# Kernel optimization log

Hardware: AMD Instinct MI355X
Metric: run time of the kernel (lower is better)

The kernel has to match this reference:

```python
import jax, jax.numpy as jnp
import numpy as np

EPS = 1e-12  # torch F.normalize default eps


def setup_inputs() -> dict:
    key = jax.random.key(0)
    k1, k2, k3, k4, k5 = jax.random.split(key, 5)
    N, E, D_IN, D_OUT = 100000, 1600000, 128, 128
    features = jax.random.normal(k1, (N, D_IN), dtype=jnp.float32)
    W = jax.random.normal(k2, (D_OUT, D_IN), dtype=jnp.float32) * 0.05
    b = jax.random.normal(k3, (D_OUT,), dtype=jnp.float32) * 0.05
    src = jax.random.randint(k4, (E,), 0, N, dtype=jnp.int32)
    dst = jax.random.randint(k5, (E,), 0, N, dtype=jnp.int32)
    return {"features": features, "W": W, "b": b, "src": src, "dst": dst}


def reference(features, W, b, src, dst):
    N = features.shape[0]
    # sum of features over each node's neighbors: scatter-add messages to dst
    neigh_sum = jax.ops.segment_sum(features[src], dst, num_segments=N)  # [N, D]
    total = jnp.sum(features, axis=0)  # [D]
    # non-neighbor sum (excl. self) + self feature == total - neighbor_sum
    h_NN = total[None, :] - neigh_sum  # [N, D]
    # row-wise L2 normalize (torch F.normalize dim=1)
    norm = jnp.sqrt(jnp.sum(h_NN * h_NN, axis=1, keepdims=True))
    h_norm = h_NN / jnp.maximum(norm, EPS)
    # linear: x @ W.T + b
    return h_norm @ W.T + b
```

## Files before the change

### kernel.cpp

```cpp
#include <hip/hip_runtime.h>
#include <hip/hip_bf16.h>

#define D 128
#define FS_CAP 5120

typedef __bf16 bf16_t;
typedef bf16_t bf16x8 __attribute__((ext_vector_type(8)));
typedef float  f32x4  __attribute__((ext_vector_type(4)));
typedef float  f32x2  __attribute__((ext_vector_type(2)));

__device__ __forceinline__ void atomAddF(float* p, float v) {
    unsafeAtomicAdd(p, v);
}

__device__ __forceinline__ uint2 pack_fp8x8(const float* v) {
    unsigned lo = 0, hi = 0;
    lo = __builtin_amdgcn_cvt_pk_fp8_f32(v[0], v[1], lo, false);
    lo = __builtin_amdgcn_cvt_pk_fp8_f32(v[2], v[3], lo, true);
    hi = __builtin_amdgcn_cvt_pk_fp8_f32(v[4], v[5], hi, false);
    hi = __builtin_amdgcn_cvt_pk_fp8_f32(v[6], v[7], hi, true);
    return make_uint2(lo, hi);
}

__device__ __forceinline__ void acc_fp8x8(uint2 w, float* acc) {
    f32x2 a = __builtin_amdgcn_cvt_pk_f32_fp8(w.x, false);
    f32x2 b = __builtin_amdgcn_cvt_pk_f32_fp8(w.x, true);
    f32x2 c = __builtin_amdgcn_cvt_pk_f32_fp8(w.y, false);
    f32x2 d = __builtin_amdgcn_cvt_pk_f32_fp8(w.y, true);
    acc[0] += a[0]; acc[1] += a[1]; acc[2] += b[0]; acc[3] += b[1];
    acc[4] += c[0]; acc[5] += c[1]; acc[6] += d[0]; acc[7] += d[1];
}

__global__ __launch_bounds__(256) void cvt_colsum_count_kernel(const float* __restrict__ feat,
                                                               uint2* __restrict__ featq,
                                                               float* __restrict__ total,
                                                               const int* __restrict__ dst,
                                                               int* __restrict__ bcount,
                                                               int* __restrict__ chunkhist,
                                                               long long n8, int nE, int NB,
                                                               int chunk) {
    __shared__ float red[4][16][8];
    __shared__ int hist[1024];
    int tid = threadIdx.x, lane = tid & 63, w = tid >> 6;
    for (int i = tid; i < NB; i += 256) hist[i] = 0;
    __syncthreads();
    long long G = (long long)gridDim.x * 256;
    float acc[8];
    #pragma unroll
    for (int e = 0; e < 8; ++e) acc[e] = 0.f;
    int c0 = blockIdx.x * chunk;
    int c1 = c0 + chunk; if (c1 > nE) c1 = nE;
    long long i = (long long)blockIdx.x * 256 + tid;
    int e = c0 + tid;
    while (i < n8 || e < c1) {
        if (i < n8) {
            const float4 a = *(const float4*)&feat[i * 8];
            const float4 b = *(const float4*)&feat[i * 8 + 4];
            float v[8] = {a.x, a.y, a.z, a.w, b.x, b.y, b.z, b.w};
            featq[i] = pack_fp8x8(v);
            acc[0] += a.x; acc[1] += a.y; acc[2] += a.z; acc[3] += a.w;
            acc[4] += b.x; acc[5] += b.y; acc[6] += b.z; acc[7] += b.w;
        }
        if (e < c1) atomicAdd(&hist[dst[e] >> 8], 1);
        i += G; e += 256;
    }
    #pragma unroll
    for (int k = 0; k < 8; ++k) {
        acc[k] += __shfl_xor(acc[k], 16, 64);
        acc[k] += __shfl_xor(acc[k], 32, 64);
    }
    if (lane < 16) {
        #pragma unroll
        for (int k = 0; k < 8; ++k) red[w][lane][k] = acc[k];
    }
    __syncthreads();
    if (tid < 128) {
        int cb = tid >> 3, k = tid & 7;
        float s = red[0][cb][k] + red[1][cb][k] + red[2][cb][k] + red[3][cb][k];
        atomAddF(&total[cb * 8 + k], s);
    }
    int* ch = chunkhist + (size_t)blockIdx.x * 1024;
    for (int k = tid; k < NB; k += 256) {
        int h = hist[k];
        ch[k] = h;
        if (h) atomicAdd(&bcount[k], h);
    }
}

__global__ __launch_bounds__(1024) void bscan_kernel(const int* __restrict__ bcount,
                                                     int* __restrict__ bbase,
                                                     int* __restrict__ bcur,
                                                     int NB, int nE) {
    int tid = threadIdx.x, lane = tid & 63, w = tid >> 6;
    int v = (tid < NB) ? bcount[tid] : 0;
    int x = v;
    #pragma unroll
    for (int off = 1; off < 64; off <<= 1) {
        int y = __shfl_up(x, off, 64);
        if (lane >= off) x += y;
    }
    __shared__ int ws[16];
    if (lane == 63) ws[w] = x;
    __syncthreads();
    if (w == 0 && lane < 16) {
        int s = ws[lane];
        #pragma unroll
        for (int off = 1; off < 16; off <<= 1) {
            int y = __shfl_up(s, off, 64);
            if (lane >= off) s += y;
        }
        ws[lane] = s;
    }
    __syncthreads();
    int base = (w == 0) ? 0 : ws[w - 1];
    int excl = base + x - v;
    if (tid < NB) { bbase[tid] = excl; bcur[tid] = excl; }
    if (tid == 0) bbase[NB] = nE;
}

__global__ __launch_bounds__(256) void bucket_scatter_kernel(const int* __restrict__ src,
                                                             const int* __restrict__ dst,
                                                             int* __restrict__ bcur,
                                                             unsigned* __restrict__ packed,
                                                             const int* __restrict__ chunkhist,
                                                             int nE, int NB, int chunk) {
    __shared__ int cur[1024];
    int tid = threadIdx.x;
    const int* ch = chunkhist + (size_t)blockIdx.x * 1024;
    for (int i = tid; i < NB; i += 256) {
        int h = ch[i];
        cur[i] = h ? atomicAdd(&bcur[i], h) : 0;
    }
    __syncthreads();
    int c0 = blockIdx.x * chunk;
    int c1 = c0 + chunk; if (c1 > nE) c1 = nE;
    for (int i = c0 + tid; i < c1; i += 256) {
        int t = dst[i];
        int b = t >> 8;
        int off = atomicAdd(&cur[b], 1);
        packed[off] = ((unsigned)(t & 255) << 17) | (unsigned)src[i];
    }
}

__global__ __launch_bounds__(1024) void fill_sort_kernel(const unsigned* __restrict__ packed,
                                                         const int* __restrict__ bbase,
                                                         int* __restrict__ ptr,
                                                         int* __restrict__ adj,
                                                         int n, int NB, int nE) {
    __shared__ int cnt[256];
    __shared__ int lcur[256];
    __shared__ int wsum[4];
    __shared__ int pbuf[FS_CAP];
    __shared__ int sbuf[FS_CAP];
    int b = blockIdx.x;
    int tid = threadIdx.x, lane = tid & 63, w = tid >> 6;
    int base = bbase[b], end = bbase[b + 1], m = end - base;
    bool fast = (m <= FS_CAP);
    if (tid < 256) cnt[tid] = 0;
    __syncthreads();
    if (fast) {
        for (int i = tid; i < m; i += 1024) {
            int pv = (int)packed[base + i];
            pbuf[i] = pv;
            atomicAdd(&cnt[pv >> 17], 1);
        }
    } else {
        for (int i = tid; i < m; i += 1024)
            atomicAdd(&cnt[packed[base + i] >> 17], 1);
    }
    __syncthreads();
    int v = 0, x = 0;
    if (tid < 256) {
        v = cnt[tid];
        x = v;
        #pragma unroll
        for (int off = 1; off < 64; off <<= 1) {
            int y = __shfl_up(x, off, 64);
            if (lane >= off) x += y;
        }
        if (lane == 63) wsum[w] = x;
    }
    __syncthreads();
    if (tid < 256) {
        int wb = 0;
        for (int k = 0; k < w; ++k) wb += wsum[k];
        int excl = wb + x - v;
        lcur[tid] = fast ? excl : base + excl;
        int node = b * 256 + tid;
        if (node < n) ptr[node] = base + excl;
    }
    if (b == NB - 1 && tid == 0) ptr[n] = nE;
    __syncthreads();
    if (fast) {
        for (int i = tid; i < m; i += 1024) {
            int pv = pbuf[i];
            int j = pv >> 17;
            int pos = atomicAdd(&lcur[j], 1);
            sbuf[pos] = pv & 0x1FFFF;
        }
        __syncthreads();
        for (int i = tid; i < m; i += 1024)
            adj[base + i] = sbuf[i];
    } else {
        for (int i = tid; i < m; i += 1024) {
            int pv = (int)packed[base + i];
            int j = pv >> 17;
            int pos = atomicAdd(&lcur[j], 1);
            adj[pos] = pv & 0x1FFFF;
        }
    }
}

__global__ __launch_bounds__(256, 4) void gather_mfma_kernel(const uint2* __restrict__ featq,
                                                             const int* __restrict__ ptr,
                                                             const int* __restrict__ adj,
                                                             const float* __restrict__ total,
                                                             const float* __restrict__ W,
                                                             const float* __restrict__ bias,
                                                             float* __restrict__ out,
                                                             int n, int ngroups) {
    __shared__ bf16_t s_hn[2][16][136];

    int tid  = threadIdx.x;
    int lane = tid & 63;
    int w    = tid >> 6;
    int quad = lane >> 4;
    int l16  = lane & 15;

    int n0 = w * 32;
    bf16x8 bfrag[4][2];
    #pragma unroll
    for (int s = 0; s < 4; ++s)
        #pragma unroll
        for (int c = 0; c < 2; ++c) {
            const float* wp = W + (size_t)(n0 + 16 * c + l16) * D + 32 * s + 8 * quad;
            float4 wa = *(const float4*)wp;
            float4 wb = *(const float4*)(wp + 4);
            bf16x8 bf;
            bf[0] = (bf16_t)wa.x; bf[1] = (bf16_t)wa.y; bf[2] = (bf16_t)wa.z; bf[3] = (bf16_t)wa.w;
            bf[4] = (bf16_t)wb.x; bf[5] = (bf16_t)wb.y; bf[6] = (bf16_t)wb.z; bf[7] = (bf16_t)wb.w;
            bfrag[s][c] = bf;
        }
    float bias0 = bias[n0 + l16];
    float bias1 = bias[n0 + 16 + l16];

    int k_node = tid >> 4;
    int d8 = (tid & 15) * 8;
    float tot8[8];
    {
        float4 ta = *(const float4*)&total[d8];
        float4 tb = *(const float4*)&total[d8 + 4];
        tot8[0] = ta.x; tot8[1] = ta.y; tot8[2] = ta.z; tot8[3] = ta.w;
        tot8[4] = tb.x; tot8[5] = tb.y; tot8[6] = tb.z; tot8[7] = tb.w;
    }

    unsigned sliceoff = (unsigned)(tid & 15) * 8;
    unsigned long long fbase = (unsigned long long)featq;
    int pb = 0;
    int gstride = gridDim.x;
    int g = blockIdx.x;

    int p0 = 0, p1 = 0, madj = 0;
    if (g < ngroups) {
        int v = g * 16 + k_node;
        if (v < n) { p0 = ptr[v]; p1 = ptr[v + 1]; }
        if (p0 < p1) { int q = p0 + l16; if (q > p1 - 1) q = p1 - 1; madj = adj[q]; }
    }

    for (; g < ngroups; g += gstride) {
        int gn = g + gstride;
        int np0 = 0, np1 = 0;
        if (gn < ngroups) {
            int vn = gn * 16 + k_node;
            if (vn < n) { np0 = ptr[vn]; np1 = ptr[vn + 1]; }
        }

        float acc8[8];
        #pragma unroll
        for (int e = 0; e < 8; ++e) acc8[e] = 0.f;

        for (int p = p0; p < p1; p += 16) {
            int rem = p1 - p;
            unsigned voff[16];
            #pragma unroll
            for (int i = 0; i < 16; ++i) {
                int idx = __shfl(madj, (lane & 48) + i, 64);
                voff[i] = ((unsigned)idx << 7) | sliceoff;
            }
            uint2 f[16];
            #pragma unroll
            for (int i = 0; i < 16; ++i)
                asm volatile("global_load_dwordx2 %0, %1, %2"
                             : "=v"(f[i]) : "v"(voff[i]), "s"(fbase));
            int adjn = 0, pn = p + 16;
            if (pn < p1) { int q = pn + l16; if (q > p1 - 1) q = p1 - 1; adjn = adj[q]; }
            asm volatile("s_waitcnt vmcnt(8)" ::: "memory");
            __builtin_amdgcn_sched_barrier(0);
            #pragma unroll
            for (int i = 0; i < 8; ++i) if (i < rem) acc_fp8x8(f[i], acc8);
            asm volatile("s_waitcnt vmcnt(0)" ::: "memory");
            __builtin_amdgcn_sched_barrier(0);
            #pragma unroll
            for (int i = 8; i < 16; ++i) if (i < rem) acc_fp8x8(f[i], acc8);
            madj = adjn;
        }

        int v = g * 16 + k_node;
        bool valid = v < n;
        float h8[8], ss = 0.f;
        #pragma unroll
        for (int e = 0; e < 8; ++e) {
            h8[e] = valid ? (tot8[e] - acc8[e]) : 0.f;
            ss = fmaf(h8[e], h8[e], ss);
        }
        ss += __shfl_xor(ss, 1, 64);
        ss += __shfl_xor(ss, 2, 64);
        ss += __shfl_xor(ss, 4, 64);
        ss += __shfl_xor(ss, 8, 64);
        float rinv = 1.0f / fmaxf(sqrtf(ss), 1e-12f);

        bf16x8 hv;
        #pragma unroll
        for (int e = 0; e < 8; ++e) hv[e] = (bf16_t)(h8[e] * rinv);
        *(bf16x8*)&s_hn[pb][k_node][d8] = hv;
        __syncthreads();

        p0 = np0; p1 = np1; madj = 0;
        if (p0 < p1) { int q = p0 + l16; if (q > p1 - 1) q = p1 - 1; madj = adj[q]; }

        f32x4 acc0 = {0.f, 0.f, 0.f, 0.f};
        f32x4 acc1 = {0.f, 0.f, 0.f, 0.f};
        #pragma unroll
        for (int s = 0; s < 4; ++s) {
            bf16x8 a = *(const bf16x8*)&s_hn[pb][l16][32 * s + 8 * quad];
            acc0 = __builtin_amdgcn_mfma_f32_16x16x32_bf16(a, bfrag[s][0], acc0, 0, 0, 0);
            acc1 = __builtin_amdgcn_mfma_f32_16x16x32_bf16(a, bfrag[s][1], acc1, 0, 0, 0);
        }
        #pragma unroll
        for (int r = 0; r < 4; ++r) {
            int row = quad * 4 + r;
            int vr = g * 16 + row;
            if (vr < n) {
                out[(size_t)vr * D + n0 + l16]      = acc0[r] + bias0;
                out[(size_t)vr * D + n0 + 16 + l16] = acc1[r] + bias1;
            }
        }
        pb ^= 1;
    }
}

__global__ __launch_bounds__(128) void col_sum_kernel(const float* __restrict__ feat,
                                                      float* __restrict__ total, int n) {
    int d = threadIdx.x;
    float acc = 0.f;
    for (int r = blockIdx.x; r < n; r += gridDim.x)
        acc += feat[(size_t)r * D + d];
    atomAddF(&total[d], acc);
}

__global__ __launch_bounds__(256) void scatter_kernel(const float* __restrict__ feat,
                                                      const int* __restrict__ src,
                                                      const int* __restrict__ dst,
                                                      float* __restrict__ neigh, int nE) {
    long long nwork = (long long)nE * 64;
    long long stride = (long long)gridDim.x * 256;
    for (long long i = (long long)blockIdx.x * 256 + threadIdx.x; i < nwork; i += stride) {
        int e = (int)(i >> 6);
        int d2 = (int)(i & 63) * 2;
        int s = src[e], t = dst[e];
        const float2 vv = *(const float2*)&feat[(size_t)s * D + d2];
        float* p = &neigh[(size_t)t * D + d2];
        atomAddF(p + 0, vv.x);
        atomAddF(p + 1, vv.y);
    }
}

__global__ __launch_bounds__(256) void finalize_kernel(const float* __restrict__ neigh,
                                                       const float* __restrict__ total,
                                                       const float* __restrict__ W,
                                                       const float* __restrict__ bias,
                                                       float* __restrict__ out,
                                                       int n, int ngroups) {
    __shared__ __hip_bfloat16 Wt[D * D];
    __shared__ __align__(16) float hnt[2][D][4];
    __shared__ float red[2][2][4];
    int tid = threadIdx.x;
    for (int idx = tid; idx < D * D; idx += 256) {
        int j = idx & 127, dd = idx >> 7;
        Wt[idx] = __float2bfloat16(W[(size_t)j * D + dd]);
    }
    int half = tid >> 7, d = tid & 127, wih = (tid >> 6) & 1, lane = tid & 63;
    float bj = bias[d], tot = total[d];
    __syncthreads();
    for (int g = blockIdx.x; g < ngroups; g += gridDim.x) {
        int nb = g * 8 + half * 4;
        float h0=0,h1=0,h2=0,h3=0;
        if (nb+0 < n) h0 = tot - neigh[(size_t)(nb+0)*D + d];
        if (nb+1 < n) h1 = tot - neigh[(size_t)(nb+1)*D + d];
        if (nb+2 < n) h2 = tot - neigh[(size_t)(nb+2)*D + d];
        if (nb+3 < n) h3 = tot - neigh[(size_t)(nb+3)*D + d];
        float s0=h0*h0,s1=h1*h1,s2=h2*h2,s3=h3*h3;
        #pragma unroll
        for (int off = 32; off > 0; off >>= 1) {
            s0 += __shfl_xor(s0, off, 64); s1 += __shfl_xor(s1, off, 64);
            s2 += __shfl_xor(s2, off, 64); s3 += __shfl_xor(s3, off, 64);
        }
        if (lane == 0) { red[half][wih][0]=s0; red[half][wih][1]=s1; red[half][wih][2]=s2; red[half][wih][3]=s3; }
        __syncthreads();
        float rinv[4];
        #pragma unroll
        for (int k = 0; k < 4; ++k)
            rinv[k] = 1.0f / fmaxf(sqrtf(red[half][0][k] + red[half][1][k]), 1e-12f);
        hnt[half][d][0]=h0*rinv[0]; hnt[half][d][1]=h1*rinv[1];
        hnt[half][d][2]=h2*rinv[2]; hnt[half][d][3]=h3*rinv[3];
        __syncthreads();
        float a0=0,a1=0,a2=0,a3=0;
        #pragma unroll 8
        for (int dd = 0; dd < D; ++dd) {
            float4 hn4 = *(const float4*)&hnt[half][dd][0];
            float wv = __bfloat162float(Wt[dd * D + d]);
            a0 = fmaf(hn4.x, wv, a0); a1 = fmaf(hn4.y, wv, a1);
            a2 = fmaf(hn4.z, wv, a2); a3 = fmaf(hn4.w, wv, a3);
        }
        if (nb+0 < n) out[(size_t)(nb+0)*D + d] = a0 + bj;
        if (nb+1 < n) out[(size_t)(nb+1)*D + d] = a1 + bj;
        if (nb+2 < n) out[(size_t)(nb+2)*D + d] = a2 + bj;
        if (nb+3 < n) out[(size_t)(nb+3)*D + d] = a3 + bj;
        __syncthreads();
    }
}

static inline size_t align_up(size_t x, size_t a) { return (x + a - 1) & ~(a - 1); }

extern "C" void kernel_launch(void* const* d_in, const int* in_sizes, int n_in,
                              void* d_out, int out_size, void* d_ws, size_t ws_size,
                              hipStream_t stream) {
    const float* feat = (const float*)d_in[0];
    const float* W    = (const float*)d_in[1];
    const float* bias = (const float*)d_in[2];
    const int*   src  = (const int*)d_in[3];
    const int*   dst  = (const int*)d_in[4];
    float* out = (float*)d_out;

    int n  = in_sizes[0] / D;
    int nE = in_sizes[3];
    int NB = (n + 255) / 256;

    char* wsb = (char*)d_ws;
    size_t o_total  = 0;
    size_t o_bcount = 512;
    size_t o_bbase  = 4608;
    size_t o_bcur   = o_bbase + 4608;
    size_t o_chist  = align_up(o_bcur + 4096, 512);
    size_t o_ptr    = o_chist + (size_t)512 * 1024 * 4;
    size_t o_adj    = align_up(o_ptr + (size_t)4 * (n + 1), 512);
    size_t o_packed = o_adj + (size_t)4 * nE;
    size_t o_featq  = align_up(o_packed + (size_t)4 * nE, 512);
    size_t needNew  = o_featq + (size_t)n * D;

    float*    total  = (float*)(wsb + o_total);
    int*      bcount = (int*)(wsb + o_bcount);
    int*      bbase  = (int*)(wsb + o_bbase);
    int*      bcur   = (int*)(wsb + o_bcur);
    int*      chist  = (int*)(wsb + o_chist);
    int*      ptr    = (int*)(wsb + o_ptr);
    int*      adj    = (int*)(wsb + o_adj);
    unsigned* packed = (unsigned*)(wsb + o_packed);
    uint2*    featq  = (uint2*)(wsb + o_featq);

    long long n8 = (long long)n * (D / 8);
    int ngroups16 = (n + 15) / 16;
    int grid16 = (ngroups16 + 2) / 3;
    if (grid16 > 4096) grid16 = 4096;

    bool packOK = (n <= (1 << 17)) && (NB <= 1024);

    if (ws_size >= needNew && packOK) {
        hipMemsetAsync(wsb, 0, o_bbase, stream);
        int chunk = (nE + 511) / 512;
        cvt_colsum_count_kernel<<<512, 256, 0, stream>>>(feat, featq, total, dst, bcount,
                                                         chist, n8, nE, NB, chunk);
        bscan_kernel<<<1, 1024, 0, stream>>>(bcount, bbase, bcur, NB, nE);
        bucket_scatter_kernel<<<512, 256, 0, stream>>>(src, dst, bcur, packed, chist,
                                                       nE, NB, chunk);
        fill_sort_kernel<<<NB, 1024, 0, stream>>>(packed, bbase, ptr, adj, n, NB, nE);
        gather_mfma_kernel<<<grid16, 256, 0, stream>>>(featq, ptr, adj, total, W,
                                                       bias, out, n, ngroups16);
    } else {
        float* neigh = out;
        if (ws_size >= D * sizeof(float))
            hipMemsetAsync(d_ws, 0, D * sizeof(float), stream);
        hipMemsetAsync(neigh, 0, (size_t)out_size * sizeof(float), stream);
        col_sum_kernel<<<512, 128, 0, stream>>>(feat, total, n);
        scatter_kernel<<<16384, 256, 0, stream>>>(feat, src, dst, neigh, nE);
        int ngroups = (n + 7) / 8;
        finalize_kernel<<<2048, 256, 0, stream>>>(neigh, total, W, bias, out, n, ngroups);
    }
}
```

Baseline: 217.8 us.

## Fold bucket prefix scan into scatter kernel and coarsen chunk histograms

Removes the single-block bscan launch by having each of 128 scatter blocks redundantly compute the bucket exclusive scan, with offsets taken from a relative cursor array. Chunk histograms are merged four-to-one with global atomics, so there are 128 larger scatter blocks of 1024 threads instead of 512 of 256. The gather kernel's grid cap and blocks-per-group ratio also change. This saves one launch and its serialization, at the cost of redundant scan work, extra atomics in the count kernel, and a larger memset region.

Result: faster. 211.5 us (-2.9%).

```diff
diff --git a/kernel.cpp b/kernel.cpp
--- a/kernel.cpp
+++ b/kernel.cpp
@@ -38,7 +38,7 @@
                                                                int* __restrict__ bcount,
                                                                int* __restrict__ chunkhist,
                                                                long long n8, int nE, int NB,
-                                                               int chunk) {
+                                                               int echunk) {
     __shared__ float red[4][16][8];
     __shared__ int hist[1024];
     int tid = threadIdx.x, lane = tid & 63, w = tid >> 6;
@@ -48,8 +48,8 @@
     float acc[8];
     #pragma unroll
     for (int e = 0; e < 8; ++e) acc[e] = 0.f;
-    int c0 = blockIdx.x * chunk;
-    int c1 = c0 + chunk; if (c1 > nE) c1 = nE;
+    int c0 = blockIdx.x * echunk;
+    int c1 = c0 + echunk; if (c1 > nE) c1 = nE;
     long long i = (long long)blockIdx.x * 256 + tid;
     int e = c0 + tid;
     while (i < n8 || e < c1) {
@@ -79,19 +79,26 @@
         float s = red[0][cb][k] + red[1][cb][k] + red[2][cb][k] + red[3][cb][k];
         atomAddF(&total[cb * 8 + k], s);
     }
-    int* ch = chunkhist + (size_t)blockIdx.x * 1024;
+    int* ch = chunkhist + (size_t)(blockIdx.x >> 2) * 1024;
     for (int k = tid; k < NB; k += 256) {
         int h = hist[k];
-        ch[k] = h;
-        if (h) atomicAdd(&bcount[k], h);
-    }
-}
-
-__global__ __launch_bounds__(1024) void bscan_kernel(const int* __restrict__ bcount,
-                                                     int* __restrict__ bbase,
-                                                     int* __restrict__ bcur,
-                                                     int NB, int nE) {
+        if (h) { atomicAdd(&ch[k], h); atomicAdd(&bcount[k], h); }
+    }
+}
+
+__global__ __launch_bounds__(1024) void bucket_scatter_kernel(const int* __restrict__ src,
+                                                              const int* __restrict__ dst,
+                                                              const int* __restrict__ bcount,
+                                                              int* __restrict__ bcur_rel,
+                                                              int* __restrict__ bbase,
+                                                              unsigned* __restrict__ packed,
+                                                              const int* __restrict__ chunkhist,
+                                                              int nE, int NB, int echunk4) {
+    __shared__ int ws[16];
+    __shared__ int cur[1024];
+    int blk = blockIdx.x;
     int tid = threadIdx.x, lane = tid & 63, w = tid >> 6;
+
     int v = (tid < NB) ? bcount[tid] : 0;
     int x = v;
     #pragma unroll
@@ -99,7 +106,6 @@
         int y = __shfl_up(x, off, 64);
         if (lane >= off) x += y;
     }
-    __shared__ int ws[16];
     if (lane == 63) ws[w] = x;
     __syncthreads();
     if (w == 0 && lane < 16) {
@@ -114,27 +120,20 @@
     __syncthreads();
     int base = (w == 0) ? 0 : ws[w - 1];
     int excl = base + x - v;
-    if (tid < NB) { bbase[tid] = excl; bcur[tid] = excl; }
-    if (tid == 0) bbase[NB] = nE;
-}
-
-__global__ __launch_bounds__(256) void bucket_scatter_kernel(const int* __restrict__ src,
-                                                             const int* __restrict__ dst,
-                                                             int* __restrict__ bcur,
-                                                             unsigned* __restrict__ packed,
-                                                             const int* __restrict__ chunkhist,
-                                                             int nE, int NB, int chunk) {
-    __shared__ int cur[1024];
-    int tid = threadIdx.x;
-    const int* ch = chunkhist + (size_t)blockIdx.x * 1024;
-    for (int i = tid; i < NB; i += 256) {
-        int h = ch[i];
-        cur[i] = h ? atomicAdd(&bcur[i], h) : 0;
-    }
-    __syncthreads();
-    int c0 = blockIdx.x * chunk;
-    int c1 = c0 + chunk; if (c1 > nE) c1 = nE;
-    for (int i = c0 + tid; i < c1; i += 256) {
+
+    if (blk == 0) {
+        if (tid < NB) bbase[tid] = excl;
+        if (tid == 0) bbase[NB] = nE;
+    }
+    if (tid < NB) {
+        int h = chunkhist[(size_t)blk * 1024 + tid];
+        cur[tid] = h ? (excl + atomicAdd(&bcur_rel[tid], h)) : 0;
+    }
+    __syncthreads();
+
+    int c0 = blk * echunk4;
+    int c1 = c0 + echunk4; if (c1 > nE) c1 = nE;
+    for (int i = c0 + tid; i < c1; i += 1024) {
         int t = dst[i];
         int b = t >> 8;
         int off = atomicAdd(&cur[b], 1);
@@ -449,10 +448,10 @@
     char* wsb = (char*)d_ws;
     size_t o_total  = 0;
     size_t o_bcount = 512;
-    size_t o_bbase  = 4608;
-    size_t o_bcur   = o_bbase + 4608;
-    size_t o_chist  = align_up(o_bcur + 4096, 512);
-    size_t o_ptr    = o_chist + (size_t)512 * 1024 * 4;
+    size_t o_bcurr  = 512 + 4096;
+    size_t o_chist  = o_bcurr + 4096;
+    size_t o_bbase  = o_chist + (size_t)128 * 1024 * 4;
+    size_t o_ptr    = align_up(o_bbase + 4608, 512);
     size_t o_adj    = align_up(o_ptr + (size_t)4 * (n + 1), 512);
     size_t o_packed = o_adj + (size_t)4 * nE;
     size_t o_featq  = align_up(o_packed + (size_t)4 * nE, 512);
@@ -460,9 +459,9 @@
 
     float*    total  = (float*)(wsb + o_total);
     int*      bcount = (int*)(wsb + o_bcount);
+    int*      bcurr  = (int*)(wsb + o_bcurr);
+    int*      chist  = (int*)(wsb + o_chist);
     int*      bbase  = (int*)(wsb + o_bbase);
-    int*      bcur   = (int*)(wsb + o_bcur);
-    int*      chist  = (int*)(wsb + o_chist);
     int*      ptr    = (int*)(wsb + o_ptr);
     int*      adj    = (int*)(wsb + o_adj);
     unsigned* packed = (unsigned*)(wsb + o_packed);
@@ -470,19 +469,19 @@
 
     long long n8 = (long long)n * (D / 8);
     int ngroups16 = (n + 15) / 16;
-    int grid16 = (ngroups16 + 2) / 3;
-    if (grid16 > 4096) grid16 = 4096;
+    int grid16 = (ngroups16 + 1) / 2;
+    if (grid16 > 16384) grid16 = 16384;
 
     bool packOK = (n <= (1 << 17)) && (NB <= 1024);
 
     if (ws_size >= needNew && packOK) {
         hipMemsetAsync(wsb, 0, o_bbase, stream);
-        int chunk = (nE + 511) / 512;
+        int echunk = (nE + 511) / 512;
+        int echunk4 = echunk * 4;
         cvt_colsum_count_kernel<<<512, 256, 0, stream>>>(feat, featq, total, dst, bcount,
-                                                         chist, n8, nE, NB, chunk);
-        bscan_kernel<<<1, 1024, 0, stream>>>(bcount, bbase, bcur, NB, nE);
-        bucket_scatter_kernel<<<512, 256, 0, stream>>>(src, dst, bcur, packed, chist,
-                                                       nE, NB, chunk);
+                                                         chist, n8, nE, NB, echunk);
+        bucket_scatter_kernel<<<128, 1024, 0, stream>>>(src, dst, bcount, bcurr, bbase,
+                                                        packed, chist, nE, NB, echunk4);
         fill_sort_kernel<<<NB, 1024, 0, stream>>>(packed, bbase, ptr, adj, n, NB, nE);
         gather_mfma_kernel<<<grid16, 256, 0, stream>>>(featq, ptr, adj, total, W,
                                                        bias, out, n, ngroups16);
```
